# Performance work log

Hardware: AMD Instinct MI355X
Metric: run time of the kernel (lower is better)

Reference implementation:

```python
import jax, jax.numpy as jnp
import numpy as np


def _sobel(img):
    # replicate-pad then Sobel cross-correlation (matches torch conv2d with wx, wy)
    p = jnp.pad(img, ((0, 0), (0, 0), (1, 1), (1, 1)), mode='edge')
    dx = ((p[:, :, 0:-2, 2:] - p[:, :, 0:-2, 0:-2])
          + 2.0 * (p[:, :, 1:-1, 2:] - p[:, :, 1:-1, 0:-2])
          + (p[:, :, 2:, 2:] - p[:, :, 2:, 0:-2]))
    dy = ((p[:, :, 2:, 0:-2] - p[:, :, 0:-2, 0:-2])
          + 2.0 * (p[:, :, 2:, 1:-1] - p[:, :, 0:-2, 1:-1])
          + (p[:, :, 2:, 2:] - p[:, :, 0:-2, 2:]))
    return dx, dy


def _compute_normal(vertex):
    # normal = normalize(dV/dx x dV/dy); zero out pixels at global min/max depth
    dx, dy = _sobel(vertex)
    n = jnp.cross(dx, dy, axis=1)                      # [B,3,H,W]
    mag = jnp.sqrt(jnp.sum(n * n, axis=1, keepdims=True) + 1e-16)
    n = n / (mag + 1e-8)
    depth = vertex[:, 2:3]
    invalid = (depth == depth.min()) | (depth == depth.max())
    return jnp.where(invalid, 0.0, n)


def _warp(feat, u, v):
    # bilinear sampling of feat [B,C,H,W] at (u,v) [B,N] -> [B,C,N]
    B, C, H, W = feat.shape
    u = jnp.clip(u, 0.0, W - 1.0)
    v = jnp.clip(v, 0.0, H - 1.0)
    u0 = jnp.floor(u); v0 = jnp.floor(v)
    wu = u - u0; wv = v - v0
    u0i = u0.astype(jnp.int32); v0i = v0.astype(jnp.int32)
    u1i = jnp.minimum(u0i + 1, W - 1); v1i = jnp.minimum(v0i + 1, H - 1)
    flat = feat.reshape(B, C, H * W)
    N = u.shape[-1]
    def g(ui, vi):
        idx = (vi * W + ui)[:, None, :]
        return jnp.take_along_axis(flat, jnp.broadcast_to(idx, (B, C, N)), axis=2)
    return (g(u0i, v0i) * ((1 - wu) * (1 - wv))[:, None]
            + g(u1i, v0i) * (wu * (1 - wv))[:, None]
            + g(u0i, v1i) * ((1 - wu) * wv)[:, None]
            + g(u1i, v1i) * (wu * wv)[:, None])


def _skew(v):  # [B,3] -> [B,3,3]
    x, y, z = v[..., 0], v[..., 1], v[..., 2]
    O = jnp.zeros_like(x)
    return jnp.stack([jnp.stack([O, -z, y], -1),
                      jnp.stack([z, O, -x], -1),
                      jnp.stack([-y, x, O], -1)], -2)


def _twist2mat(w):  # Rodrigues: so(3) [B,3] -> SO(3) [B,3,3]
    th = jnp.sqrt(jnp.sum(w * w, -1, keepdims=True) + 1e-24)
    Kv = _skew(w / th)
    th = th[..., None]
    I = jnp.eye(3, dtype=w.dtype)
    return I + jnp.sin(th) * Kv + (1.0 - jnp.cos(th)) * (Kv @ Kv)


def _icp_forward(depth0, depth1, K, R, t, max_iter=3):
    B, _, H, W = depth0.shape
    fx, fy, cx, cy = [K[:, i:i + 1] for i in range(4)]  # each [B,1]
    uu = jnp.arange(W, dtype=depth0.dtype)
    vv = jnp.arange(H, dtype=depth0.dtype)
    px = (uu[None, None, None, :] - cx[:, :, None, None]) / fx[:, :, None, None]
    py = (vv[None, None, :, None] - cy[:, :, None, None]) / fy[:, :, None, None]
    px = jnp.broadcast_to(px, (B, 1, H, W))
    py = jnp.broadcast_to(py, (B, 1, H, W))
    vertex0 = jnp.concatenate([px * depth0, py * depth0, depth0], 1)  # [B,3,H,W]
    vertex1 = jnp.concatenate([px * depth1, py * depth1, depth1], 1)
    normal0 = _compute_normal(vertex0)
    normal1 = _compute_normal(vertex1)
    N = H * W
    V0 = vertex0.reshape(B, 3, N)
    N0 = normal0.reshape(B, 3, N)
    P0 = V0.transpose(0, 2, 1)                          # [B,N,3]
    dpt0 = vertex0[:, 2].reshape(B, N)
    sigma_z = 0.0012 + 0.0019 * (dpt0 - 0.4) ** 2       # depth noise model
    eye6 = jnp.eye(6, dtype=depth0.dtype)
    for _ in range(max_iter):
        v0to1 = R @ V0 + t                               # [B,3,N]
        x_, y_, s_ = v0to1[:, 0], v0to1[:, 1], v0to1[:, 2]
        u_ = x_ / s_ * fx + cx
        v_ = y_ / s_ * fy + cy
        inviews = (u_ > 0) & (u_ < W - 1) & (v_ > 0) & (v_ < H - 1)
        rV1 = _warp(vertex1, u_, v_)                     # [B,3,N]
        rN1 = _warp(normal1, u_, v_)
        diff = v0to1 - rV1
        dnorm = jnp.sqrt(jnp.sum(diff * diff, axis=1) + 1e-16)
        occ = (~inviews) | (dnorm > 0.1)                 # [B,N]
        res = jnp.sum(rN1 * diff, axis=1)                # point-to-plane residual [B,N]
        NtC = jnp.einsum('bcn,bck->bnk', rN1, R)         # n_r^T R, [B,N,3]
        # n^T [p]_x == cross(n^T R, p)
        J = jnp.concatenate([jnp.cross(NtC, P0), -NtC], -1)  # [B,N,6]
        # sigma ~ |n_r . (R e_z)| * sigma_z (depth noise projected on normal)
        ndot = jnp.abs(jnp.sum(rN1 * R[:, :, 2][:, :, None], axis=1))
        sigma = ndot * sigma_z + 1e-3
        w_res = res / (sigma + 1e-8)
        J = -J / (sigma + 1e-8)[..., None]
        w_res = jnp.where(occ, 0.0, w_res)
        J = jnp.where(occ[..., None], 0.0, J)
        JtWJ = jnp.einsum('bnk,bnl->bkl', J, J)          # [B,6,6]
        JtR = jnp.einsum('bnk,bn->bk', J, w_res)[..., None]  # [B,6,1]
        tr = jnp.trace(JtWJ, axis1=1, axis2=2)
        Hlm = JtWJ + (tr * 1e-6)[:, None, None] * eye6   # LM damping
        xi = jnp.linalg.inv(Hlm) @ JtR                   # [B,6,1]
        dR = _twist2mat(-xi[:, :3, 0])
        dt = -(dR @ xi[:, 3:])
        R, t = R @ dR, R @ dt + t                        # inverse-compositional update
    weights = jnp.ones((B, 1, H, W), dtype=depth0.dtype)
    return R, t, weights


def setup_inputs() -> dict:
    key = jax.random.key(0)
    B, H, W = 16, 480, 640
    k1, k2, k3, k4 = jax.random.split(key, 4)
    TWO_PI = 6.2831853
    xs = jnp.linspace(0.0, 1.0, W, dtype=jnp.float32)
    ys = jnp.linspace(0.0, 1.0, H, dtype=jnp.float32)
    phase = jax.random.uniform(k1, (B, 1, 1, 1), minval=0.0, maxval=TWO_PI)
    # smooth positive depth surface so ICP inlier test keeps valid pixels
    depth0 = (2.0 + 0.5 * jnp.sin(TWO_PI * 3.0 * xs[None, None, None, :] + phase)
              * jnp.cos(TWO_PI * 2.0 * ys[None, None, :, None])).astype(jnp.float32)
    depth1 = depth0 + 0.01 * jax.random.normal(k2, (B, 1, H, W), dtype=jnp.float32)
    K = jnp.tile(jnp.array([[525.0, 525.0, 319.5, 239.5]], dtype=jnp.float32), (B, 1))
    w = 0.005 * jax.random.normal(k3, (B, 3), dtype=jnp.float32)
    R = _twist2mat(w)                                    # near-identity initial rotation
    t = 0.005 * jax.random.normal(k4, (B, 3, 1), dtype=jnp.float32)
    return {"depth0": depth0, "depth1": depth1, "K": K, "R": R, "t": t}


def reference(depth0, depth1, K, R, t):
    return _icp_forward(depth0, depth1, K, R, t, max_iter=3)
```

## Files before the change

### kernel.cpp

```cpp
#include <hip/hip_runtime.h>

#define IMH 480
#define IMW 640
#define HW (IMH*IMW)
#define NB 16

#define PPT 12
#define BPB 100
#define STRIDE_PX (BPB*256)
#define STRIDE_ROWS (STRIDE_PX/IMW)

__device__ inline unsigned fenc(float x){
    unsigned u = __float_as_uint(x);
    return (u & 0x80000000u) ? ~u : (u | 0x80000000u);
}
__device__ inline float fdec(unsigned e){
    unsigned u = (e & 0x80000000u) ? (e & 0x7FFFFFFFu) : ~e;
    return __uint_as_float(u);
}

__global__ void init_kernel(const float* __restrict__ Rin, const float* __restrict__ tin,
                            float* __restrict__ stateR, float* __restrict__ statet,
                            unsigned* __restrict__ mm, float* __restrict__ acc){
    int i = threadIdx.x;
    if (i < NB*9) stateR[i] = Rin[i];
    if (i < NB*3) statet[i] = tin[i];
    if (i == 0){ mm[0] = 0xFFFFFFFFu; mm[1] = 0u; }
    for (int k = i; k < NB*27; k += 256) acc[k] = 0.f;
}

__global__ __launch_bounds__(256) void minmax_kernel(const float4* __restrict__ d, unsigned* __restrict__ mm){
    unsigned lmin = 0xFFFFFFFFu, lmax = 0u;
    const int total4 = NB*HW/4;
    for (int i = blockIdx.x*256 + threadIdx.x; i < total4; i += gridDim.x*256){
        float4 v = d[i];
        unsigned e0 = fenc(v.x), e1 = fenc(v.y), e2 = fenc(v.z), e3 = fenc(v.w);
        lmin = min(lmin, min(min(e0,e1), min(e2,e3)));
        lmax = max(lmax, max(max(e0,e1), max(e2,e3)));
    }
    #pragma unroll
    for (int off = 32; off; off >>= 1){
        lmin = min(lmin, (unsigned)__shfl_down((int)lmin, off));
        lmax = max(lmax, (unsigned)__shfl_down((int)lmax, off));
    }
    __shared__ unsigned smin[4], smax[4];
    int wave = threadIdx.x >> 6, lane = threadIdx.x & 63;
    if (lane == 0){ smin[wave] = lmin; smax[wave] = lmax; }
    __syncthreads();
    if (threadIdx.x == 0){
        unsigned bmin = min(min(smin[0],smin[1]), min(smin[2],smin[3]));
        unsigned bmax = max(max(smax[0],smax[1]), max(smax[2],smax[3]));
        atomicMin(&mm[0], bmin);
        atomicMax(&mm[1], bmax);
    }
}

__global__ __launch_bounds__(256) void normal_kernel(const float* __restrict__ depth1,
                                                     const float* __restrict__ Kp,
                                                     const unsigned* __restrict__ mm,
                                                     float* __restrict__ normal1,
                                                     float* __restrict__ weights){
    int b = blockIdx.y;
    int pix = blockIdx.x*256 + threadIdx.x;
    int r = pix / IMW, c = pix % IMW;
    const float fx = Kp[b*4+0], fy = Kp[b*4+1], cx = Kp[b*4+2], cy = Kp[b*4+3];
    const float inv_fx = 1.f/fx, inv_fy = 1.f/fy;
    const float* __restrict__ d = depth1 + (size_t)b*HW;
    int rm = max(r-1,0), rp = min(r+1,IMH-1), cm = max(c-1,0), cp = min(c+1,IMW-1);

    auto vert = [&](int rr, int cc, float v[3]){
        float dd = d[rr*IMW+cc];
        v[0] = ((float)cc - cx)*inv_fx*dd;
        v[1] = ((float)rr - cy)*inv_fy*dd;
        v[2] = dd;
    };
    float va[3],vb[3],vc2[3],vd[3],ve[3],vf[3],vg[3],vh[3];
    vert(rm,cm,va); vert(rm,c,vb);  vert(rm,cp,vc2);
    vert(r ,cm,vd);                 vert(r ,cp,ve);
    vert(rp,cm,vf); vert(rp,c,vg);  vert(rp,cp,vh);

    float dx[3], dy[3];
    #pragma unroll
    for (int k=0;k<3;k++){
        dx[k] = (vc2[k]-va[k]) + 2.f*(ve[k]-vd[k]) + (vh[k]-vf[k]);
        dy[k] = (vf[k]-va[k]) + 2.f*(vg[k]-vb[k]) + (vh[k]-vc2[k]);
    }
    float nx = dx[1]*dy[2] - dx[2]*dy[1];
    float ny = dx[2]*dy[0] - dx[0]*dy[2];
    float nz = dx[0]*dy[1] - dx[1]*dy[0];
    float mag = sqrtf(nx*nx + ny*ny + nz*nz + 1e-16f);
    float inv = __builtin_amdgcn_rcpf(mag + 1e-8f);
    nx *= inv; ny *= inv; nz *= inv;

    float dc = d[r*IMW+c];
    float dmin = fdec(mm[0]), dmax = fdec(mm[1]);
    if (dc == dmin || dc == dmax){ nx = 0.f; ny = 0.f; nz = 0.f; }

    size_t base = ((size_t)b*HW + pix)*3;
    normal1[base+0] = nx;
    normal1[base+1] = ny;
    normal1[base+2] = nz;
    weights[(size_t)b*HW + pix] = 1.f;
}

__global__ __launch_bounds__(256) void iter_kernel(const float* __restrict__ depth0,
                                                   const float* __restrict__ depth1,
                                                   const float* __restrict__ normal1,
                                                   const float* __restrict__ Kp,
                                                   const float* __restrict__ stateR,
                                                   const float* __restrict__ statet,
                                                   float* __restrict__ acc){
    const int b = blockIdx.y;
    const float fx = Kp[b*4+0], fy = Kp[b*4+1], cx = Kp[b*4+2], cy = Kp[b*4+3];
    const float inv_fx = 1.f/fx, inv_fy = 1.f/fy;
    float Rm[9];
    #pragma unroll
    for (int i=0;i<9;i++) Rm[i] = stateR[b*9+i];
    float tv[3];
    #pragma unroll
    for (int i=0;i<3;i++) tv[i] = statet[b*3+i];

    const float* __restrict__ d0p = depth0 + (size_t)b*HW;
    const float* __restrict__ d1  = depth1 + (size_t)b*HW;
    const float* __restrict__ nbs = normal1 + (size_t)b*HW*3;

    float accv[27];
    #pragma unroll
    for (int i=0;i<27;i++) accv[i] = 0.f;

    const int tid = blockIdx.x*256 + threadIdx.x;
    const int c  = tid % IMW;
    const int r0 = tid / IMW;
    const float px0 = ((float)c - cx)*inv_fx;
    float py = ((float)r0 - cy)*inv_fy;
    const float py_step = (float)STRIDE_ROWS*inv_fy;

    int pix = tid;

    #pragma unroll 1
    for (int pp = 0; pp < PPT; pp++){
        float d0 = d0p[pix];
        float V0x = px0*d0;
        float V0y = py*d0;
        float V0z = d0;

        float X = Rm[0]*V0x + Rm[1]*V0y + Rm[2]*V0z + tv[0];
        float Y = Rm[3]*V0x + Rm[4]*V0y + Rm[5]*V0z + tv[1];
        float Z = Rm[6]*V0x + Rm[7]*V0y + Rm[8]*V0z + tv[2];
        float invZ = __builtin_amdgcn_rcpf(Z);
        float uu = X*invZ*fx + cx;
        float vv = Y*invZ*fy + cy;

        bool inview = (uu > 0.f) && (uu < (float)(IMW-1)) && (vv > 0.f) && (vv < (float)(IMH-1));

        float J0=0.f,J1=0.f,J2=0.f,J3=0.f,J4=0.f,J5=0.f,wres=0.f;
        if (inview){
            float u0f = floorf(uu), v0f = floorf(vv);
            int u0 = (int)u0f, v0 = (int)v0f;
            float wu = uu - u0f, wv = vv - v0f;
            float w00 = (1.f-wu)*(1.f-wv), w10 = wu*(1.f-wv), w01 = (1.f-wu)*wv, w11 = wu*wv;
            int i00 = v0*IMW + u0;

            float d00 = d1[i00], d10 = d1[i00+1], d01 = d1[i00+IMW], d11 = d1[i00+IMW+1];
            float pxa = (u0f - cx)*inv_fx, pxb = pxa + inv_fx;
            float pya = (v0f - cy)*inv_fy, pyb = pya + inv_fy;
            float a = w00*d00, bb = w10*d10, cc = w01*d01, ee = w11*d11;
            float rVz = (a + bb) + (cc + ee);
            float rVx = (a + cc)*pxa + (bb + ee)*pxb;
            float rVy = (a + bb)*pya + (cc + ee)*pyb;

            const float* __restrict__ n00 = nbs + (size_t)i00*3;
            const float* __restrict__ n01 = nbs + (size_t)(i00+IMW)*3;
            float n0x = w00*n00[0] + w10*n00[3] + w01*n01[0] + w11*n01[3];
            float n0y = w00*n00[1] + w10*n00[4] + w01*n01[1] + w11*n01[4];
            float n0z = w00*n00[2] + w10*n00[5] + w01*n01[2] + w11*n01[5];

            float dfx = X - rVx, dfy = Y - rVy, dfz = Z - rVz;
            float d2 = dfx*dfx + dfy*dfy + dfz*dfz + 1e-16f;
            if (d2 <= 0.01f){
                float res = n0x*dfx + n0y*dfy + n0z*dfz;
                float N0 = n0x*Rm[0] + n0y*Rm[3] + n0z*Rm[6];
                float N1 = n0x*Rm[1] + n0y*Rm[4] + n0z*Rm[7];
                float N2 = n0x*Rm[2] + n0y*Rm[5] + n0z*Rm[8];
                float c0 = N1*V0z - N2*V0y;
                float c1 = N2*V0x - N0*V0z;
                float c2 = N0*V0y - N1*V0x;
                float ndot = fabsf(N2);
                float dsh = d0 - 0.4f;
                float sigz = 0.0012f + 0.0019f*dsh*dsh;
                float sigma = ndot*sigz + 0.001f;
                float invs = __builtin_amdgcn_rcpf(sigma + 1e-8f);
                wres = res*invs;
                J0 = -c0*invs; J1 = -c1*invs; J2 = -c2*invs;
                J3 =  N0*invs; J4 =  N1*invs; J5 =  N2*invs;
            }
        }

        float Jv[6] = {J0,J1,J2,J3,J4,J5};
        int idx = 0;
        #pragma unroll
        for (int k=0;k<6;k++)
            #pragma unroll
            for (int l=k;l<6;l++){ accv[idx] += Jv[k]*Jv[l]; idx++; }
        #pragma unroll
        for (int k=0;k<6;k++){ accv[idx] += Jv[k]*wres; idx++; }

        pix += STRIDE_PX;
        py  += py_step;
    }

    #pragma unroll
    for (int i=0;i<27;i++){
        float v = accv[i];
        #pragma unroll
        for (int off=32; off; off >>= 1) v += __shfl_down(v, off);
        accv[i] = v;
    }

    __shared__ float sacc[4][27];
    int wave = threadIdx.x >> 6, lane = threadIdx.x & 63;
    if (lane == 0){
        #pragma unroll
        for (int i=0;i<27;i++) sacc[wave][i] = accv[i];
    }
    __syncthreads();
    if (threadIdx.x < 27){
        float s = sacc[0][threadIdx.x] + sacc[1][threadIdx.x]
                + sacc[2][threadIdx.x] + sacc[3][threadIdx.x];
        atomicAdd(&acc[b*27 + threadIdx.x], s);
    }
}

__global__ void solve_kernel(float* __restrict__ acc,
                             float* __restrict__ stateR, float* __restrict__ statet,
                             float* __restrict__ outR, float* __restrict__ outt){
    int b = threadIdx.x;
    if (b >= NB) return;

    float a27[27];
    for (int i=0;i<27;i++) a27[i] = acc[b*27+i];
    for (int i=0;i<27;i++) acc[b*27+i] = 0.f;

    double A[6][6], rhs[6];
    int idx = 0;
    for (int k=0;k<6;k++)
        for (int l=k;l<6;l++){ A[k][l] = a27[idx]; A[l][k] = a27[idx]; idx++; }
    for (int k=0;k<6;k++) rhs[k] = a27[21+k];

    double tr = 0.0;
    for (int k=0;k<6;k++) tr += A[k][k];
    double lm = tr*1e-6;
    for (int k=0;k<6;k++) A[k][k] += lm;

    double M[6][7];
    for (int i=0;i<6;i++){ for (int j=0;j<6;j++) M[i][j]=A[i][j]; M[i][6]=rhs[i]; }
    for (int col=0; col<6; col++){
        int piv = col; double best = fabs(M[col][col]);
        for (int r2=col+1; r2<6; r2++){
            double v = fabs(M[r2][col]);
            if (v > best){ best = v; piv = r2; }
        }
        if (piv != col)
            for (int j=0;j<7;j++){ double tmp = M[col][j]; M[col][j] = M[piv][j]; M[piv][j] = tmp; }
        double p = M[col][col];
        for (int j=col;j<7;j++) M[col][j] /= p;
        for (int r2=0;r2<6;r2++){
            if (r2 == col) continue;
            double f = M[r2][col];
            for (int j=col;j<7;j++) M[r2][j] -= f*M[col][j];
        }
    }
    double xi[6];
    for (int k=0;k<6;k++) xi[k] = M[k][6];

    double w0 = -xi[0], w1 = -xi[1], w2 = -xi[2];
    double th = sqrt(w0*w0 + w1*w1 + w2*w2 + 1e-24);
    double kx = w0/th, ky = w1/th, kz = w2/th;
    double s = sin(th), cm1 = 1.0 - cos(th);
    double Kv[3][3] = {{0,-kz,ky},{kz,0,-kx},{-ky,kx,0}};
    double K2[3][3];
    for (int i=0;i<3;i++)
        for (int j=0;j<3;j++){
            double acc2 = 0.0;
            for (int k=0;k<3;k++) acc2 += Kv[i][k]*Kv[k][j];
            K2[i][j] = acc2;
        }
    double dR[3][3];
    for (int i=0;i<3;i++)
        for (int j=0;j<3;j++)
            dR[i][j] = (i==j ? 1.0 : 0.0) + s*Kv[i][j] + cm1*K2[i][j];
    double dt[3];
    for (int i=0;i<3;i++)
        dt[i] = -(dR[i][0]*xi[3] + dR[i][1]*xi[4] + dR[i][2]*xi[5]);

    double Ro[3][3];
    for (int i=0;i<3;i++) for (int j=0;j<3;j++) Ro[i][j] = (double)stateR[b*9 + i*3 + j];
    double to[3];
    for (int i=0;i<3;i++) to[i] = (double)statet[b*3+i];

    double Rn[3][3], tn[3];
    for (int i=0;i<3;i++)
        for (int j=0;j<3;j++){
            double acc2 = 0.0;
            for (int k=0;k<3;k++) acc2 += Ro[i][k]*dR[k][j];
            Rn[i][j] = acc2;
        }
    for (int i=0;i<3;i++)
        tn[i] = Ro[i][0]*dt[0] + Ro[i][1]*dt[1] + Ro[i][2]*dt[2] + to[i];

    for (int i=0;i<3;i++)
        for (int j=0;j<3;j++){
            float v = (float)Rn[i][j];
            stateR[b*9 + i*3 + j] = v;
            outR[b*9 + i*3 + j] = v;
        }
    for (int i=0;i<3;i++){
        float v = (float)tn[i];
        statet[b*3+i] = v;
        outt[b*3+i] = v;
    }
}

extern "C" void kernel_launch(void* const* d_in, const int* in_sizes, int n_in,
                              void* d_out, int out_size, void* d_ws, size_t ws_size,
                              hipStream_t stream){
    const float* depth0 = (const float*)d_in[0];
    const float* depth1 = (const float*)d_in[1];
    const float* Kp     = (const float*)d_in[2];
    const float* Rin    = (const float*)d_in[3];
    const float* tin    = (const float*)d_in[4];

    float* out     = (float*)d_out;
    float* outR    = out;
    float* outt    = out + NB*9;
    float* weights = out + NB*12;

    float* normal1 = (float*)d_ws;
    float* stateR  = normal1 + (size_t)3*NB*HW;
    float* statet  = stateR + NB*9;
    unsigned* mm   = (unsigned*)(statet + NB*3);
    float* acc     = (float*)(mm + 2);

    init_kernel<<<1, 256, 0, stream>>>(Rin, tin, stateR, statet, mm, acc);
    minmax_kernel<<<dim3(256), 256, 0, stream>>>((const float4*)depth1, mm);
    normal_kernel<<<dim3(HW/256, NB), 256, 0, stream>>>(depth1, Kp, mm, normal1, weights);
    for (int it = 0; it < 3; it++){
        iter_kernel<<<dim3(BPB, NB), 256, 0, stream>>>(depth0, depth1, normal1, Kp, stateR, statet, acc);
        solve_kernel<<<1, 64, 0, stream>>>(acc, stateR, statet, outR, outt);
    }
}
```

Baseline: 273.4 us.

## Store normals as packed fp16 and vectorize depth0 loads in ICP iterations

Normals are now stored as packed half2 pairs in an 8-byte aligned uint2 per pixel instead of three fp32 floats. Each bilinear tap becomes a single aligned 8-byte load, and both the normal-kernel write traffic and the per-iteration gather traffic shrink. The iteration kernel also gives each thread four contiguous pixels, loaded as one float4 of depth0, in place of one strided pixel per step. Normals lose precision to fp16 rounding, which could shift the residuals and Jacobians slightly.

Measured after the change: 251.9 us. 1.09x faster.

```diff
diff --git a/kernel.cpp b/kernel.cpp
--- a/kernel.cpp
+++ b/kernel.cpp
@@ -1,14 +1,17 @@
 #include <hip/hip_runtime.h>
+#include <hip/hip_fp16.h>
 
 #define IMH 480
 #define IMW 640
 #define HW (IMH*IMW)
 #define NB 16
 
-#define PPT 12
 #define BPB 100
-#define STRIDE_PX (BPB*256)
-#define STRIDE_ROWS (STRIDE_PX/IMW)
+#define TPX 4
+#define GROUPS 3
+#define THREADS_PB (BPB*256)
+#define GSTRIDE (THREADS_PB*TPX)
+#define GROWS (GSTRIDE/IMW)
 
 __device__ inline unsigned fenc(float x){
     unsigned u = __float_as_uint(x);
@@ -58,7 +61,7 @@
 __global__ __launch_bounds__(256) void normal_kernel(const float* __restrict__ depth1,
                                                      const float* __restrict__ Kp,
                                                      const unsigned* __restrict__ mm,
-                                                     float* __restrict__ normal1,
+                                                     uint2* __restrict__ nrm,
                                                      float* __restrict__ weights){
     int b = blockIdx.y;
     int pix = blockIdx.x*256 + threadIdx.x;
@@ -96,16 +99,18 @@
     float dmin = fdec(mm[0]), dmax = fdec(mm[1]);
     if (dc == dmin || dc == dmax){ nx = 0.f; ny = 0.f; nz = 0.f; }
 
-    size_t base = ((size_t)b*HW + pix)*3;
-    normal1[base+0] = nx;
-    normal1[base+1] = ny;
-    normal1[base+2] = nz;
+    __half2 hxy = __floats2half2_rn(nx, ny);
+    __half2 hz0 = __floats2half2_rn(nz, 0.f);
+    uint2 p;
+    p.x = *reinterpret_cast<unsigned*>(&hxy);
+    p.y = *reinterpret_cast<unsigned*>(&hz0);
+    nrm[(size_t)b*HW + pix] = p;
     weights[(size_t)b*HW + pix] = 1.f;
 }
 
-__global__ __launch_bounds__(256) void iter_kernel(const float* __restrict__ depth0,
+__global__ __launch_bounds__(256) void iter_kernel(const float4* __restrict__ depth0_v4,
                                                    const float* __restrict__ depth1,
-                                                   const float* __restrict__ normal1,
+                                                   const uint2* __restrict__ nrm,
                                                    const float* __restrict__ Kp,
                                                    const float* __restrict__ stateR,
                                                    const float* __restrict__ statet,
@@ -120,93 +125,106 @@
     #pragma unroll
     for (int i=0;i<3;i++) tv[i] = statet[b*3+i];
 
-    const float* __restrict__ d0p = depth0 + (size_t)b*HW;
-    const float* __restrict__ d1  = depth1 + (size_t)b*HW;
-    const float* __restrict__ nbs = normal1 + (size_t)b*HW*3;
+    const float4* __restrict__ d0v = depth0_v4 + (size_t)b*(HW/4);
+    const float* __restrict__ d1   = depth1 + (size_t)b*HW;
+    const uint2* __restrict__ nb_  = nrm + (size_t)b*HW;
 
     float accv[27];
     #pragma unroll
     for (int i=0;i<27;i++) accv[i] = 0.f;
 
     const int tid = blockIdx.x*256 + threadIdx.x;
-    const int c  = tid % IMW;
-    const int r0 = tid / IMW;
-    const float px0 = ((float)c - cx)*inv_fx;
-    float py = ((float)r0 - cy)*inv_fy;
-    const float py_step = (float)STRIDE_ROWS*inv_fy;
-
-    int pix = tid;
+    const int base0 = tid*TPX;
+    const int c0 = base0 % IMW;
+    const int r0 = base0 / IMW;
+    const float px_base = ((float)c0 - cx)*inv_fx;
+    float pyv = ((float)r0 - cy)*inv_fy;
+    const float py_step = (float)GROWS*inv_fy;
 
     #pragma unroll 1
-    for (int pp = 0; pp < PPT; pp++){
-        float d0 = d0p[pix];
-        float V0x = px0*d0;
-        float V0y = py*d0;
-        float V0z = d0;
-
-        float X = Rm[0]*V0x + Rm[1]*V0y + Rm[2]*V0z + tv[0];
-        float Y = Rm[3]*V0x + Rm[4]*V0y + Rm[5]*V0z + tv[1];
-        float Z = Rm[6]*V0x + Rm[7]*V0y + Rm[8]*V0z + tv[2];
-        float invZ = __builtin_amdgcn_rcpf(Z);
-        float uu = X*invZ*fx + cx;
-        float vv = Y*invZ*fy + cy;
-
-        bool inview = (uu > 0.f) && (uu < (float)(IMW-1)) && (vv > 0.f) && (vv < (float)(IMH-1));
-
-        float J0=0.f,J1=0.f,J2=0.f,J3=0.f,J4=0.f,J5=0.f,wres=0.f;
-        if (inview){
-            float u0f = floorf(uu), v0f = floorf(vv);
-            int u0 = (int)u0f, v0 = (int)v0f;
-            float wu = uu - u0f, wv = vv - v0f;
-            float w00 = (1.f-wu)*(1.f-wv), w10 = wu*(1.f-wv), w01 = (1.f-wu)*wv, w11 = wu*wv;
-            int i00 = v0*IMW + u0;
-
-            float d00 = d1[i00], d10 = d1[i00+1], d01 = d1[i00+IMW], d11 = d1[i00+IMW+1];
-            float pxa = (u0f - cx)*inv_fx, pxb = pxa + inv_fx;
-            float pya = (v0f - cy)*inv_fy, pyb = pya + inv_fy;
-            float a = w00*d00, bb = w10*d10, cc = w01*d01, ee = w11*d11;
-            float rVz = (a + bb) + (cc + ee);
-            float rVx = (a + cc)*pxa + (bb + ee)*pxb;
-            float rVy = (a + bb)*pya + (cc + ee)*pyb;
-
-            const float* __restrict__ n00 = nbs + (size_t)i00*3;
-            const float* __restrict__ n01 = nbs + (size_t)(i00+IMW)*3;
-            float n0x = w00*n00[0] + w10*n00[3] + w01*n01[0] + w11*n01[3];
-            float n0y = w00*n00[1] + w10*n00[4] + w01*n01[1] + w11*n01[4];
-            float n0z = w00*n00[2] + w10*n00[5] + w01*n01[2] + w11*n01[5];
-
-            float dfx = X - rVx, dfy = Y - rVy, dfz = Z - rVz;
-            float d2 = dfx*dfx + dfy*dfy + dfz*dfz + 1e-16f;
-            if (d2 <= 0.01f){
-                float res = n0x*dfx + n0y*dfy + n0z*dfz;
-                float N0 = n0x*Rm[0] + n0y*Rm[3] + n0z*Rm[6];
-                float N1 = n0x*Rm[1] + n0y*Rm[4] + n0z*Rm[7];
-                float N2 = n0x*Rm[2] + n0y*Rm[5] + n0z*Rm[8];
-                float c0 = N1*V0z - N2*V0y;
-                float c1 = N2*V0x - N0*V0z;
-                float c2 = N0*V0y - N1*V0x;
-                float ndot = fabsf(N2);
-                float dsh = d0 - 0.4f;
-                float sigz = 0.0012f + 0.0019f*dsh*dsh;
-                float sigma = ndot*sigz + 0.001f;
-                float invs = __builtin_amdgcn_rcpf(sigma + 1e-8f);
-                wres = res*invs;
-                J0 = -c0*invs; J1 = -c1*invs; J2 = -c2*invs;
-                J3 =  N0*invs; J4 =  N1*invs; J5 =  N2*invs;
+    for (int g = 0; g < GROUPS; g++){
+        float4 d4 = d0v[tid + g*THREADS_PB];
+        float dd[4] = {d4.x, d4.y, d4.z, d4.w};
+
+        #pragma unroll
+        for (int j = 0; j < TPX; j++){
+            float d0 = dd[j];
+            float V0x = (px_base + (float)j*inv_fx)*d0;
+            float V0y = pyv*d0;
+            float V0z = d0;
+
+            float X = Rm[0]*V0x + Rm[1]*V0y + Rm[2]*V0z + tv[0];
+            float Y = Rm[3]*V0x + Rm[4]*V0y + Rm[5]*V0z + tv[1];
+            float Z = Rm[6]*V0x + Rm[7]*V0y + Rm[8]*V0z + tv[2];
+            float invZ = __builtin_amdgcn_rcpf(Z);
+            float uu = X*invZ*fx + cx;
+            float vv = Y*invZ*fy + cy;
+
+            bool inview = (uu > 0.f) && (uu < (float)(IMW-1)) && (vv > 0.f) && (vv < (float)(IMH-1));
+
+            float J0=0.f,J1=0.f,J2=0.f,J3=0.f,J4=0.f,J5=0.f,wres=0.f;
+            if (inview){
+                float u0f = floorf(uu), v0f = floorf(vv);
+                int u0 = (int)u0f, v0 = (int)v0f;
+                float wu = uu - u0f, wv = vv - v0f;
+                float w00 = (1.f-wu)*(1.f-wv), w10 = wu*(1.f-wv), w01 = (1.f-wu)*wv, w11 = wu*wv;
+                int i00 = v0*IMW + u0;
+
+                float d00 = d1[i00], d10 = d1[i00+1], d01 = d1[i00+IMW], d11 = d1[i00+IMW+1];
+                uint2 h00 = nb_[i00], h10 = nb_[i00+1], h01 = nb_[i00+IMW], h11 = nb_[i00+IMW+1];
+
+                float pxa = (u0f - cx)*inv_fx, pxb = pxa + inv_fx;
+                float pya = (v0f - cy)*inv_fy, pyb = pya + inv_fy;
+                float a = w00*d00, bb = w10*d10, cc = w01*d01, ee = w11*d11;
+                float rVz = (a + bb) + (cc + ee);
+                float rVx = (a + cc)*pxa + (bb + ee)*pxb;
+                float rVy = (a + bb)*pya + (cc + ee)*pyb;
+
+                float2 n00xy = __half22float2(*reinterpret_cast<__half2*>(&h00.x));
+                float2 n00z_ = __half22float2(*reinterpret_cast<__half2*>(&h00.y));
+                float2 n10xy = __half22float2(*reinterpret_cast<__half2*>(&h10.x));
+                float2 n10z_ = __half22float2(*reinterpret_cast<__half2*>(&h10.y));
+                float2 n01xy = __half22float2(*reinterpret_cast<__half2*>(&h01.x));
+                float2 n01z_ = __half22float2(*reinterpret_cast<__half2*>(&h01.y));
+                float2 n11xy = __half22float2(*reinterpret_cast<__half2*>(&h11.x));
+                float2 n11z_ = __half22float2(*reinterpret_cast<__half2*>(&h11.y));
+
+                float n0x = w00*n00xy.x + w10*n10xy.x + w01*n01xy.x + w11*n11xy.x;
+                float n0y = w00*n00xy.y + w10*n10xy.y + w01*n01xy.y + w11*n11xy.y;
+                float n0z = w00*n00z_.x + w10*n10z_.x + w01*n01z_.x + w11*n11z_.x;
+
+                float dfx = X - rVx, dfy = Y - rVy, dfz = Z - rVz;
+                float d2 = dfx*dfx + dfy*dfy + dfz*dfz + 1e-16f;
+                if (d2 <= 0.01f){
+                    float res = n0x*dfx + n0y*dfy + n0z*dfz;
+                    float N0 = n0x*Rm[0] + n0y*Rm[3] + n0z*Rm[6];
+                    float N1 = n0x*Rm[1] + n0y*Rm[4] + n0z*Rm[7];
+                    float N2 = n0x*Rm[2] + n0y*Rm[5] + n0z*Rm[8];
+                    float cr0 = N1*V0z - N2*V0y;
+                    float cr1 = N2*V0x - N0*V0z;
+                    float cr2 = N0*V0y - N1*V0x;
+                    float ndot = fabsf(N2);
+                    float dsh = d0 - 0.4f;
+                    float sigz = 0.0012f + 0.0019f*dsh*dsh;
+                    float sigma = ndot*sigz + 0.001f;
+                    float invs = __builtin_amdgcn_rcpf(sigma + 1e-8f);
+                    wres = res*invs;
+                    J0 = -cr0*invs; J1 = -cr1*invs; J2 = -cr2*invs;
+                    J3 =  N0*invs;  J4 =  N1*invs;  J5 =  N2*invs;
+                }
             }
-        }
-
-        float Jv[6] = {J0,J1,J2,J3,J4,J5};
-        int idx = 0;
-        #pragma unroll
-        for (int k=0;k<6;k++)
+
+            float Jv[6] = {J0,J1,J2,J3,J4,J5};
+            int idx = 0;
             #pragma unroll
-            for (int l=k;l<6;l++){ accv[idx] += Jv[k]*Jv[l]; idx++; }
-        #pragma unroll
-        for (int k=0;k<6;k++){ accv[idx] += Jv[k]*wres; idx++; }
-
-        pix += STRIDE_PX;
-        py  += py_step;
+            for (int k=0;k<6;k++)
+                #pragma unroll
+                for (int l=k;l<6;l++){ accv[idx] += Jv[k]*Jv[l]; idx++; }
+            #pragma unroll
+            for (int k=0;k<6;k++){ accv[idx] += Jv[k]*wres; idx++; }
+        }
+
+        pyv += py_step;
     }
 
     #pragma unroll
@@ -335,17 +353,17 @@
     float* outt    = out + NB*9;
     float* weights = out + NB*12;
 
-    float* normal1 = (float*)d_ws;
-    float* stateR  = normal1 + (size_t)3*NB*HW;
+    uint2* nrm     = (uint2*)d_ws;
+    float* stateR  = (float*)(nrm + (size_t)NB*HW);
     float* statet  = stateR + NB*9;
     unsigned* mm   = (unsigned*)(statet + NB*3);
     float* acc     = (float*)(mm + 2);
 
     init_kernel<<<1, 256, 0, stream>>>(Rin, tin, stateR, statet, mm, acc);
     minmax_kernel<<<dim3(256), 256, 0, stream>>>((const float4*)depth1, mm);
-    normal_kernel<<<dim3(HW/256, NB), 256, 0, stream>>>(depth1, Kp, mm, normal1, weights);
+    normal_kernel<<<dim3(HW/256, NB), 256, 0, stream>>>(depth1, Kp, mm, nrm, weights);
     for (int it = 0; it < 3; it++){
-        iter_kernel<<<dim3(BPB, NB), 256, 0, stream>>>(depth0, depth1, normal1, Kp, stateR, statet, acc);
+        iter_kernel<<<dim3(BPB, NB), 256, 0, stream>>>((const float4*)depth0, depth1, nrm, Kp, stateR, statet, acc);
         solve_kernel<<<1, 64, 0, stream>>>(acc, stateR, statet, outR, outt);
     }
 }
```
